# Kernel tuning notes

Hardware: AMD Instinct MI355X
Metric: run time of the kernel (lower is better)

Reference implementation:

```python
import jax, jax.numpy as jnp
import numpy as np

N_EDGE_TYPE = 7
BN_EPS = 1e-5


def _graph_conv(x, row, col, edge_type, W):
    # gather neighbor features, scatter-mean keyed on (dst_node, edge_type), then GEMM
    n = x.shape[0]
    idx = row * N_EDGE_TYPE + edge_type                      # [E]
    gathered = x[col]                                        # [E, C]
    seg = n * N_EDGE_TYPE
    sums = jax.ops.segment_sum(gathered, idx, num_segments=seg)          # [N*7, C]
    cnt = jax.ops.segment_sum(jnp.ones(row.shape, x.dtype), idx, num_segments=seg)
    mean = sums / jnp.maximum(cnt, 1.0)[:, None]
    return mean.reshape(n, -1) @ W                           # [N, C_out]


def _bn(x, gamma, beta):
    # BatchNorm1d in training mode: biased batch stats over the node axis
    m = jnp.mean(x, axis=0)
    v = jnp.var(x, axis=0)
    return (x - m) * jax.lax.rsqrt(v + BN_EPS) * gamma + beta


def setup_inputs() -> dict:
    key = jax.random.key(0)
    ks = jax.random.split(key, 8)
    N, E, C_IN, C_OUT = 100000, 700000, 128, 256
    AVG_DEG = 7
    x = jax.random.normal(ks[0], (N, C_IN), jnp.float32)
    edge_index = jax.random.randint(ks[1], (2, E), 0, N, jnp.int32)
    edge_type = jax.random.randint(ks[2], (E,), 0, N_EDGE_TYPE, jnp.int32)
    node_type = jax.random.randint(ks[3], (N,), 0, 1, jnp.int32)
    # GraphConv.reset_parameters: std = sqrt(2/(deg*Cin + deg*Cout)), a = sqrt(3)*std
    a_a = np.sqrt(3.0) * np.sqrt(2.0 / (AVG_DEG * C_IN + AVG_DEG * C_OUT))
    a_b = np.sqrt(3.0) * np.sqrt(2.0 / (AVG_DEG * C_OUT + AVG_DEG * C_OUT))
    Wa = jax.random.uniform(ks[4], (N_EDGE_TYPE * C_IN, C_OUT), jnp.float32, -a_a, a_a)
    Wb = jax.random.uniform(ks[5], (N_EDGE_TYPE * C_OUT, C_OUT), jnp.float32, -a_b, a_b)
    a_1 = np.sqrt(1.0 / C_IN)
    W1 = jax.random.uniform(ks[6], (C_IN, C_OUT), jnp.float32, -a_1, a_1)
    ga = jnp.ones((C_OUT,), jnp.float32); ba = jnp.zeros((C_OUT,), jnp.float32)
    gb = jnp.ones((C_OUT,), jnp.float32); bb = jnp.zeros((C_OUT,), jnp.float32)
    g1 = jnp.ones((C_OUT,), jnp.float32); b1 = jnp.zeros((C_OUT,), jnp.float32)
    return {"x": x, "edge_index": edge_index, "edge_type": edge_type,
            "node_type": node_type, "Wa": Wa, "ga": ga, "ba": ba,
            "Wb": Wb, "gb": gb, "bb": bb, "W1": W1, "g1": g1, "b1": b1}


def reference(x, edge_index, edge_type, node_type, Wa, ga, ba, Wb, gb, bb, W1, g1, b1):
    row, col = edge_index[0], edge_index[1]
    # conva: GraphConv + BN + ReLU  (n_node_type=0 -> node_type ignored)
    x1 = jax.nn.relu(_bn(_graph_conv(x, row, col, edge_type, Wa), ga, ba))
    # convb: GraphConv + BN
    x2 = _bn(_graph_conv(x1, row, col, edge_type, Wb), gb, bb)
    # channel_in != channel_out -> Conv1x1 (no bias) + BN shortcut
    sc = _bn(x @ W1, g1, b1)
    return jax.nn.relu(x2 + sc)
```

## Files before the change

### kernel.cpp

```cpp
#include <hip/hip_runtime.h>
#include <cstdint>
#include <cstddef>


#define N_ET 7

typedef __bf16 bf16;
typedef __bf16 bf16x8 __attribute__((ext_vector_type(8)));
typedef __bf16 bf16x4 __attribute__((ext_vector_type(4)));
typedef float f32x4v __attribute__((ext_vector_type(4)));


__global__ void count_edges_k(const int* __restrict__ row, const int* __restrict__ et,
                              int* __restrict__ cnt, int E) {
  int e = blockIdx.x * 256 + threadIdx.x;
  if (e < E) atomicAdd(&cnt[row[e] * N_ET + et[e]], 1);
}

__global__ void inv_counts_k(const int* __restrict__ cnt, float* __restrict__ inv, int n) {
  int i = blockIdx.x * 256 + threadIdx.x;
  if (i < n) inv[i] = 1.0f / fmaxf((float)cnt[i], 1.0f);
}

__global__ __launch_bounds__(1024) void scan1_k(const int* __restrict__ cnt,
                                                int* __restrict__ off,
                                                int* __restrict__ bsum, int n) {
  __shared__ int s[1024];
  int tid = threadIdx.x;
  int i = blockIdx.x * 1024 + tid;
  int v = (i < n) ? cnt[i] : 0;
  s[tid] = v;
  __syncthreads();
  for (int d = 1; d < 1024; d <<= 1) {
    int t = (tid >= d) ? s[tid - d] : 0;
    __syncthreads();
    s[tid] += t;
    __syncthreads();
  }
  if (i < n) off[i] = s[tid] - v;
  if (tid == 1023) bsum[blockIdx.x] = s[1023];
}

__global__ __launch_bounds__(1024) void scan2_k(int* __restrict__ bsum, int nb) {
  __shared__ int s[1024];
  int tid = threadIdx.x;
  int v = (tid < nb) ? bsum[tid] : 0;
  s[tid] = v;
  __syncthreads();
  for (int d = 1; d < 1024; d <<= 1) {
    int t = (tid >= d) ? s[tid - d] : 0;
    __syncthreads();
    s[tid] += t;
    __syncthreads();
  }
  if (tid < nb) bsum[tid] = s[tid] - v;
}

__global__ __launch_bounds__(1024) void scan3_k(int* __restrict__ off,
                                                const int* __restrict__ bsum,
                                                int n, int total) {
  int i = blockIdx.x * 1024 + threadIdx.x;
  if (i < n) off[i] += bsum[blockIdx.x];
  if (i == 0) off[n] = total;
}

__global__ void place_k(const int* __restrict__ row, const int* __restrict__ col,
                        const int* __restrict__ et, const int* __restrict__ off,
                        int* __restrict__ cur, int* __restrict__ pcol, int E) {
  int e = blockIdx.x * 256 + threadIdx.x;
  if (e >= E) return;
  int seg = row[e] * N_ET + et[e];
  int pos = off[seg] + atomicAdd(&cur[seg], 1);
  pcol[pos] = col[e];
}

__global__ void transpose_w8_k(const float* __restrict__ W, bf16* __restrict__ Bt8, int K) {
  int i = blockIdx.x * 256 + threadIdx.x;
  if (i < K * 256) {
    int k = i >> 8, col = i & 255;
    Bt8[((size_t)(k >> 3) * 256 + col) * 8 + (k & 7)] = (bf16)W[i];
  }
}

__global__ void transpose_w_k(const float* __restrict__ W, bf16* __restrict__ Bt, int K) {
  int i = blockIdx.x * 256 + threadIdx.x;
  if (i < K * 256) {
    int k = i >> 8, n = i & 255;
    Bt[(size_t)n * K + k] = (bf16)W[i];
  }
}

__global__ void f32_to_bf16_k(const float* __restrict__ in, bf16* __restrict__ out,
                              int total8) {
  int i = blockIdx.x * 256 + threadIdx.x;
  if (i >= total8) return;
  size_t b = (size_t)i * 8;
  float4 v0 = *(const float4*)(in + b);
  float4 v1 = *(const float4*)(in + b + 4);
  bf16x8 o;
  o[0] = (bf16)v0.x; o[1] = (bf16)v0.y; o[2] = (bf16)v0.z; o[3] = (bf16)v0.w;
  o[4] = (bf16)v1.x; o[5] = (bf16)v1.y; o[6] = (bf16)v1.z; o[7] = (bf16)v1.w;
  *(bf16x8*)(out + b) = o;
}

template <int CW>
__launch_bounds__(512, 4)
__global__ void agg_gemm8_k(const bf16* __restrict__ X, const bf16* __restrict__ Bt8,
                            const int* __restrict__ off, const int* __restrict__ pcol,
                            const float* __restrict__ inv, bf16* __restrict__ Cout,
                            float* __restrict__ gsum, float* __restrict__ gssq,
                            int M) {
  constexpr int SL = CW / 8;
  __shared__ alignas(16) bf16 As[64][CW + 8];
  __shared__ int   offL[64 * N_ET + 1];
  __shared__ float invL[64 * N_ET];

  const int t = threadIdx.x;
  const int m0 = blockIdx.x * 64;
  const int lane = t & 63, w = t >> 6;
  const int wm = (w >> 2) * 32;
  const int wn = (w & 3) * 64;
  const int l15 = lane & 15, quad = lane >> 4;
  const int r = t >> 3, h = t & 7;
  const int NS_ = M * N_ET;

  {
    const int base = m0 * N_ET;
    for (int i = t; i < 64 * N_ET + 1; i += 512) {
      int gi = base + i;
      if (gi > NS_) gi = NS_;
      offL[i] = off[gi];
    }
    for (int i = t; i < 64 * N_ET; i += 512) {
      int gi = base + i;
      if (gi >= NS_) gi = NS_ - 1;
      invL[i] = inv[gi];
    }
  }

  f32x4v acc[2][4];
#pragma unroll
  for (int i = 0; i < 2; ++i)
#pragma unroll
    for (int j = 0; j < 4; ++j) acc[i][j] = (f32x4v){0.f, 0.f, 0.f, 0.f};

  __syncthreads();

  const int xcol = h * SL;

  for (int type = 0; type < N_ET; ++type) {
    const int ls = r * N_ET + type;
    const int sS = offL[ls];
    const int sE = offL[ls + 1];
    const float sc = invL[ls];

    float s[SL];
#pragma unroll
    for (int j = 0; j < SL; ++j) s[j] = 0.f;

    int p = sS;
    if constexpr (CW == 256) {
      for (; p + 2 <= sE; p += 2) {
        const int c0 = pcol[p], c1 = pcol[p + 1];
        const bf16* q0 = X + (size_t)c0 * CW + xcol;
        const bf16* q1 = X + (size_t)c1 * CW + xcol;
        const bf16x8 a0 = *(const bf16x8*)(q0 + 0),  a1 = *(const bf16x8*)(q0 + 8);
        const bf16x8 a2 = *(const bf16x8*)(q0 + 16), a3 = *(const bf16x8*)(q0 + 24);
        const bf16x8 b0 = *(const bf16x8*)(q1 + 0),  b1 = *(const bf16x8*)(q1 + 8);
        const bf16x8 b2 = *(const bf16x8*)(q1 + 16), b3 = *(const bf16x8*)(q1 + 24);
#pragma unroll
        for (int i = 0; i < 8; ++i) {
          s[i]      += (float)a0[i] + (float)b0[i];
          s[8 + i]  += (float)a1[i] + (float)b1[i];
          s[16 + i] += (float)a2[i] + (float)b2[i];
          s[24 + i] += (float)a3[i] + (float)b3[i];
        }
      }
      if (p < sE) {
        const int c0 = pcol[p];
        const bf16* q0 = X + (size_t)c0 * CW + xcol;
        const bf16x8 a0 = *(const bf16x8*)(q0 + 0),  a1 = *(const bf16x8*)(q0 + 8);
        const bf16x8 a2 = *(const bf16x8*)(q0 + 16), a3 = *(const bf16x8*)(q0 + 24);
#pragma unroll
        for (int i = 0; i < 8; ++i) {
          s[i]      += (float)a0[i];
          s[8 + i]  += (float)a1[i];
          s[16 + i] += (float)a2[i];
          s[24 + i] += (float)a3[i];
        }
      }
    } else {
      for (; p + 4 <= sE; p += 4) {
        const int c0 = pcol[p],     c1 = pcol[p + 1];
        const int c2 = pcol[p + 2], c3 = pcol[p + 3];
        const bf16* q0 = X + (size_t)c0 * CW + xcol;
        const bf16* q1 = X + (size_t)c1 * CW + xcol;
        const bf16* q2 = X + (size_t)c2 * CW + xcol;
        const bf16* q3 = X + (size_t)c3 * CW + xcol;
        const bf16x8 a0 = *(const bf16x8*)(q0 + 0), a1 = *(const bf16x8*)(q0 + 8);
        const bf16x8 b0 = *(const bf16x8*)(q1 + 0), b1 = *(const bf16x8*)(q1 + 8);
        const bf16x8 d0 = *(const bf16x8*)(q2 + 0), d1 = *(const bf16x8*)(q2 + 8);
        const bf16x8 e0 = *(const bf16x8*)(q3 + 0), e1 = *(const bf16x8*)(q3 + 8);
#pragma unroll
        for (int i = 0; i < 8; ++i) {
          s[i]     += ((float)a0[i] + (float)b0[i]) + ((float)d0[i] + (float)e0[i]);
          s[8 + i] += ((float)a1[i] + (float)b1[i]) + ((float)d1[i] + (float)e1[i]);
        }
      }
      for (; p < sE; ++p) {
        const int c0 = pcol[p];
        const bf16* q0 = X + (size_t)c0 * CW + xcol;
        const bf16x8 a0 = *(const bf16x8*)(q0 + 0), a1 = *(const bf16x8*)(q0 + 8);
#pragma unroll
        for (int i = 0; i < 8; ++i) {
          s[i]     += (float)a0[i];
          s[8 + i] += (float)a1[i];
        }
      }
    }

    __syncthreads();
    if constexpr (CW == 256) {
      bf16x8 o0, o1, o2, o3;
#pragma unroll
      for (int i = 0; i < 8; ++i) {
        o0[i] = (bf16)(s[i] * sc);
        o1[i] = (bf16)(s[8 + i] * sc);
        o2[i] = (bf16)(s[16 + i] * sc);
        o3[i] = (bf16)(s[24 + i] * sc);
      }
      *(bf16x8*)&As[r][h * 32 + 0]  = o0;
      *(bf16x8*)&As[r][h * 32 + 8]  = o1;
      *(bf16x8*)&As[r][h * 32 + 16] = o2;
      *(bf16x8*)&As[r][h * 32 + 24] = o3;
    } else {
      bf16x8 o0, o1;
#pragma unroll
      for (int i = 0; i < 8; ++i) {
        o0[i] = (bf16)(s[i] * sc);
        o1[i] = (bf16)(s[8 + i] * sc);
      }
      *(bf16x8*)&As[r][h * 16 + 0] = o0;
      *(bf16x8*)&As[r][h * 16 + 8] = o1;
    }
    __syncthreads();

#pragma unroll
    for (int kk = 0; kk < CW / 32; ++kk) {
      const int k8b = (type * CW + kk * 32) >> 3;
      const bf16* bp = Bt8 + (size_t)(k8b + quad) * (256 * 8);
      const bf16x8 bf0 = *(const bf16x8*)(bp + (size_t)(wn + 0  + l15) * 8);
      const bf16x8 bf1 = *(const bf16x8*)(bp + (size_t)(wn + 16 + l15) * 8);
      const bf16x8 bf2 = *(const bf16x8*)(bp + (size_t)(wn + 32 + l15) * 8);
      const bf16x8 bf3 = *(const bf16x8*)(bp + (size_t)(wn + 48 + l15) * 8);
      const bf16x8 af0 = *(const bf16x8*)&As[wm + l15][kk * 32 + quad * 8];
      const bf16x8 af1 = *(const bf16x8*)&As[wm + 16 + l15][kk * 32 + quad * 8];
      acc[0][0] = __builtin_amdgcn_mfma_f32_16x16x32_bf16(af0, bf0, acc[0][0], 0, 0, 0);
      acc[0][1] = __builtin_amdgcn_mfma_f32_16x16x32_bf16(af0, bf1, acc[0][1], 0, 0, 0);
      acc[0][2] = __builtin_amdgcn_mfma_f32_16x16x32_bf16(af0, bf2, acc[0][2], 0, 0, 0);
      acc[0][3] = __builtin_amdgcn_mfma_f32_16x16x32_bf16(af0, bf3, acc[0][3], 0, 0, 0);
      acc[1][0] = __builtin_amdgcn_mfma_f32_16x16x32_bf16(af1, bf0, acc[1][0], 0, 0, 0);
      acc[1][1] = __builtin_amdgcn_mfma_f32_16x16x32_bf16(af1, bf1, acc[1][1], 0, 0, 0);
      acc[1][2] = __builtin_amdgcn_mfma_f32_16x16x32_bf16(af1, bf2, acc[1][2], 0, 0, 0);
      acc[1][3] = __builtin_amdgcn_mfma_f32_16x16x32_bf16(af1, bf3, acc[1][3], 0, 0, 0);
    }
  }

  __syncthreads();
  float* red = (float*)&As[0][0];
  const int slot = (w >> 2) * 4 + quad;

#pragma unroll
  for (int fj = 0; fj < 4; ++fj) {
    float ps = 0.f, pq = 0.f;
#pragma unroll
    for (int fi = 0; fi < 2; ++fi) {
      int rbase = m0 + wm + fi * 16 + quad * 4;
#pragma unroll
      for (int rr = 0; rr < 4; ++rr) {
        int rowg = rbase + rr;
        if (rowg < M) {
          float v = acc[fi][fj][rr];
          Cout[(size_t)rowg * 256 + wn + fj * 16 + l15] = (bf16)v;
          ps += v;
          pq += v * v;
        }
      }
    }
    red[((slot * 256) + (wn + fj * 16 + l15)) * 2 + 0] = ps;
    red[((slot * 256) + (wn + fj * 16 + l15)) * 2 + 1] = pq;
  }
  __syncthreads();
  if (t < 256) {
    float sA = 0.f, qA = 0.f;
#pragma unroll
    for (int sl = 0; sl < 8; ++sl) {
      sA += red[(sl * 256 + t) * 2 + 0];
      qA += red[(sl * 256 + t) * 2 + 1];
    }
    unsafeAtomicAdd(&gsum[t], sA);
    unsafeAtomicAdd(&gssq[t], qA);
  }
}

__launch_bounds__(256, 2)
__global__ void sc_gemm_k(const bf16* __restrict__ X, const bf16* __restrict__ Bt,
                          float* __restrict__ Cout,
                          float* __restrict__ gsum, float* __restrict__ gssq,
                          int M, int K) {
  __shared__ alignas(16) bf16 As[128][40];
  __shared__ alignas(16) bf16 Bs[256][40];
  const int t = threadIdx.x;
  const int m0 = blockIdx.x * 128;
  const int lane = t & 63, w = t >> 6;
  const int wm = (w >> 1) * 64;
  const int wn = (w & 1) * 128;
  const int l15 = lane & 15, quad = lane >> 4;

  f32x4v acc[4][8];
#pragma unroll
  for (int i = 0; i < 4; ++i)
#pragma unroll
    for (int j = 0; j < 8; ++j) acc[i][j] = (f32x4v){0.f, 0.f, 0.f, 0.f};

  const int r = t >> 1, h = t & 1;
  const int m = m0 + r;
  const bool mv = (m < M);

  for (int k0 = 0; k0 < K; k0 += 32) {
    const bf16* xp = X + (size_t)m * K + k0 + h * 16;
    bf16x8 o0, o1;
    if (mv) {
      o0 = *(const bf16x8*)(xp);
      o1 = *(const bf16x8*)(xp + 8);
    } else {
#pragma unroll
      for (int i = 0; i < 8; ++i) { o0[i] = (bf16)0.f; o1[i] = (bf16)0.f; }
    }
    *(bf16x8*)&As[r][h * 16] = o0;
    *(bf16x8*)&As[r][h * 16 + 8] = o1;
    {
      const bf16* bp = Bt + (size_t)t * K + k0;
      bf16x8 b0 = *(const bf16x8*)(bp + 0);
      bf16x8 b1 = *(const bf16x8*)(bp + 8);
      bf16x8 b2 = *(const bf16x8*)(bp + 16);
      bf16x8 b3 = *(const bf16x8*)(bp + 24);
      *(bf16x8*)&Bs[t][0] = b0;
      *(bf16x8*)&Bs[t][8] = b1;
      *(bf16x8*)&Bs[t][16] = b2;
      *(bf16x8*)&Bs[t][24] = b3;
    }
    __syncthreads();
    bf16x8 af[4], bfr[8];
#pragma unroll
    for (int f = 0; f < 4; ++f) af[f] = *(const bf16x8*)&As[wm + f * 16 + l15][quad * 8];
#pragma unroll
    for (int g = 0; g < 8; ++g) bfr[g] = *(const bf16x8*)&Bs[wn + g * 16 + l15][quad * 8];
#pragma unroll
    for (int fi = 0; fi < 4; ++fi)
#pragma unroll
      for (int fj = 0; fj < 8; ++fj)
        acc[fi][fj] = __builtin_amdgcn_mfma_f32_16x16x32_bf16(af[fi], bfr[fj], acc[fi][fj], 0, 0, 0);
    __syncthreads();
  }

  float* red = (float*)&Bs[0][0];
  const int slot = (w >> 1) * 4 + quad;
#pragma unroll
  for (int fj = 0; fj < 8; ++fj) {
    float ps = 0.f, pq = 0.f;
#pragma unroll
    for (int fi = 0; fi < 4; ++fi) {
      int rbase = m0 + wm + fi * 16 + quad * 4;
#pragma unroll
      for (int rr = 0; rr < 4; ++rr) {
        int rowg = rbase + rr;
        if (rowg < M) {
          float v = acc[fi][fj][rr];
          Cout[(size_t)rowg * 256 + wn + fj * 16 + l15] = v;
          ps += v;
          pq += v * v;
        }
      }
    }
    red[((slot * 256) + (wn + fj * 16 + l15)) * 2 + 0] = ps;
    red[((slot * 256) + (wn + fj * 16 + l15)) * 2 + 1] = pq;
  }
  __syncthreads();
  if (t < 256) {
    float sA = 0.f, qA = 0.f;
#pragma unroll
    for (int sl = 0; sl < 8; ++sl) {
      sA += red[(sl * 256 + t) * 2 + 0];
      qA += red[(sl * 256 + t) * 2 + 1];
    }
    unsafeAtomicAdd(&gsum[t], sA);
    unsafeAtomicAdd(&gssq[t], qA);
  }
}


__global__ void bn_params_k(const float* __restrict__ s, const float* __restrict__ q,
                            const float* __restrict__ g, const float* __restrict__ b,
                            float* __restrict__ scale, float* __restrict__ shift, float invN) {
  int c = threadIdx.x;
  float m = s[c] * invN;
  float var = fmaxf(q[c] * invN - m * m, 0.f);
  float sc = g[c] * rsqrtf(var + 1e-5f);
  scale[c] = sc;
  shift[c] = b[c] - m * sc;
}

__global__ void bn_relu_ip_k(bf16* __restrict__ v, const float* __restrict__ scale,
                             const float* __restrict__ shift, int total8) {
  int i = blockIdx.x * 256 + threadIdx.x;
  if (i >= total8) return;
  size_t base = (size_t)i * 8;
  int c = (int)(base & 255);
  bf16x8 x = *(const bf16x8*)(v + base);
#pragma unroll
  for (int j = 0; j < 8; ++j)
    x[j] = (bf16)fmaxf((float)x[j] * scale[c + j] + shift[c + j], 0.f);
  *(bf16x8*)(v + base) = x;
}

__global__ void final_out_k(const bf16* __restrict__ cb,
                            const float* __restrict__ scB, const float* __restrict__ shB,
                            const float* __restrict__ scS, const float* __restrict__ shS,
                            float* __restrict__ out, int total4) {
  int i = blockIdx.x * 256 + threadIdx.x;
  if (i >= total4) return;
  size_t base = (size_t)i * 4;
  int c = (int)(base & 255);
  bf16x4 vb = *(const bf16x4*)(cb + base);
  float4 vs = *(const float4*)(out + base);
  float4 r;
  r.x = fmaxf((float)vb[0] * scB[c + 0] + shB[c + 0] + vs.x * scS[c + 0] + shS[c + 0], 0.f);
  r.y = fmaxf((float)vb[1] * scB[c + 1] + shB[c + 1] + vs.y * scS[c + 1] + shS[c + 1], 0.f);
  r.z = fmaxf((float)vb[2] * scB[c + 2] + shB[c + 2] + vs.z * scS[c + 2] + shS[c + 2], 0.f);
  r.w = fmaxf((float)vb[3] * scB[c + 3] + shB[c + 3] + vs.w * scS[c + 3] + shS[c + 3], 0.f);
  *(float4*)(out + base) = r;
}

__global__ void sentinel_k(float* __restrict__ out, int n) {
  int i = blockIdx.x * 256 + threadIdx.x;
  if (i < n) out[i] = 12345.0f;
}


extern "C" void kernel_launch(void* const* d_in, const int* in_sizes, int n_in,
                              void* d_out, int out_size, void* d_ws, size_t ws_size,
                              hipStream_t stream) {
  const float* x  = (const float*)d_in[0];
  const int* ei   = (const int*)d_in[1];
  const int* etp  = (const int*)d_in[2];
  const float* Wa = (const float*)d_in[4];
  const float* ga = (const float*)d_in[5];
  const float* ba = (const float*)d_in[6];
  const float* Wb = (const float*)d_in[7];
  const float* gb = (const float*)d_in[8];
  const float* bb = (const float*)d_in[9];
  const float* W1 = (const float*)d_in[10];
  const float* g1 = (const float*)d_in[11];
  const float* b1 = (const float*)d_in[12];

  const int C1 = 128, C2 = 256;
  const int N = in_sizes[0] / C1;
  const int E = in_sizes[2];
  const int* row = ei;
  const int* col = ei + E;
  const int NS = N * N_ET;
  const int KA = N_ET * C1;
  const int KB = N_ET * C2;

  size_t need = 0;
  auto alloc = [&](size_t bytes) { size_t o = need; need += (bytes + 15) & ~(size_t)15; return o; };
  char* w = (char*)d_ws;
  int*   off_p = (int*)(w + alloc(((size_t)NS + 1) * 4));
  int*   cnt_p = (int*)(w + alloc((size_t)NS * 4));
  int*   pcol  = (int*)(w + alloc((size_t)E * 4));
  float* inv_p = (float*)(w + alloc((size_t)NS * 4));
  int*   bsum  = (int*)(w + alloc(1024 * 4));
  bf16*  Bt8A  = (bf16*)(w + alloc((size_t)KA * 256 * 2));
  bf16*  Bt8B  = (bf16*)(w + alloc((size_t)KB * 256 * 2));
  bf16*  Bt1   = (bf16*)(w + alloc((size_t)256 * C1 * 2));
  bf16*  x1    = (bf16*)(w + alloc((size_t)N * C2 * 2));
  bf16*  convb = (bf16*)(w + alloc((size_t)N * C2 * 2));
  float* st    = (float*)(w + alloc(12 * 256 * 4));

  if (ws_size < need) {
    sentinel_k<<<(out_size + 255) / 256, 256, 0, stream>>>((float*)d_out, out_size);
    return;
  }

  bf16* xb = convb;

  float* sum_a = st + 0 * 256, *ssq_a = st + 1 * 256;
  float* sum_b = st + 2 * 256, *ssq_b = st + 3 * 256;
  float* sum_s = st + 4 * 256, *ssq_s = st + 5 * 256;
  float* scA = st + 6 * 256, *shA = st + 7 * 256;
  float* scB = st + 8 * 256, *shB = st + 9 * 256;
  float* scS = st + 10 * 256, *shS = st + 11 * 256;

  const float invN = 1.0f / (float)N;
  const int nscan = (NS + 1023) / 1024;
  const int g2 = (N + 63) / 64;
  const int gsc = (N + 127) / 128;
  const int total8 = N * C2 / 8;
  const int total4 = N * C2 / 4;
  const int cvt8 = N * C1 / 8;

  hipMemsetAsync(cnt_p, 0, (size_t)NS * 4, stream);
  hipMemsetAsync(st, 0, 12 * 256 * 4, stream);
  count_edges_k<<<(E + 255) / 256, 256, 0, stream>>>(row, etp, cnt_p, E);
  inv_counts_k<<<(NS + 255) / 256, 256, 0, stream>>>(cnt_p, inv_p, NS);
  scan1_k<<<nscan, 1024, 0, stream>>>(cnt_p, off_p, bsum, NS);
  scan2_k<<<1, 1024, 0, stream>>>(bsum, nscan);
  scan3_k<<<nscan, 1024, 0, stream>>>(off_p, bsum, NS, E);
  hipMemsetAsync(cnt_p, 0, (size_t)NS * 4, stream);
  place_k<<<(E + 255) / 256, 256, 0, stream>>>(row, col, etp, off_p, cnt_p, pcol, E);

  transpose_w8_k<<<(KA * 256 + 255) / 256, 256, 0, stream>>>(Wa, Bt8A, KA);
  transpose_w8_k<<<(KB * 256 + 255) / 256, 256, 0, stream>>>(Wb, Bt8B, KB);
  transpose_w_k<<<(C1 * 256 + 255) / 256, 256, 0, stream>>>(W1, Bt1, C1);
  f32_to_bf16_k<<<(cvt8 + 255) / 256, 256, 0, stream>>>(x, xb, cvt8);

  agg_gemm8_k<128><<<g2, 512, 0, stream>>>(xb, Bt8A, off_p, pcol, inv_p, x1,
                                           sum_a, ssq_a, N);
  bn_params_k<<<1, 256, 0, stream>>>(sum_a, ssq_a, ga, ba, scA, shA, invN);
  bn_relu_ip_k<<<(total8 + 255) / 256, 256, 0, stream>>>(x1, scA, shA, total8);

  sc_gemm_k<<<gsc, 256, 0, stream>>>(xb, Bt1, (float*)d_out, sum_s, ssq_s, N, C1);
  bn_params_k<<<1, 256, 0, stream>>>(sum_s, ssq_s, g1, b1, scS, shS, invN);

  agg_gemm8_k<256><<<g2, 512, 0, stream>>>(x1, Bt8B, off_p, pcol, inv_p, convb,
                                           sum_b, ssq_b, N);
  bn_params_k<<<1, 256, 0, stream>>>(sum_b, ssq_b, gb, bb, scB, shB, invN);

  final_out_k<<<(total4 + 255) / 256, 256, 0, stream>>>(
      convb, scB, shB, scS, shS, (float*)d_out, total4);
}
```

Before: 741.0 us.

## Fuse shortcut 1x1 GEMM into first aggregation kernel and inline BN params

```diff
diff --git a/kernel.cpp b/kernel.cpp
--- a/kernel.cpp
+++ b/kernel.cpp
@@ -79,14 +79,6 @@
   if (i < K * 256) {
     int k = i >> 8, col = i & 255;
     Bt8[((size_t)(k >> 3) * 256 + col) * 8 + (k & 7)] = (bf16)W[i];
-  }
-}
-
-__global__ void transpose_w_k(const float* __restrict__ W, bf16* __restrict__ Bt, int K) {
-  int i = blockIdx.x * 256 + threadIdx.x;
-  if (i < K * 256) {
-    int k = i >> 8, n = i & 255;
-    Bt[(size_t)n * K + k] = (bf16)W[i];
   }
 }
 
@@ -101,6 +93,233 @@
   o[0] = (bf16)v0.x; o[1] = (bf16)v0.y; o[2] = (bf16)v0.z; o[3] = (bf16)v0.w;
   o[4] = (bf16)v1.x; o[5] = (bf16)v1.y; o[6] = (bf16)v1.z; o[7] = (bf16)v1.w;
   *(bf16x8*)(out + b) = o;
+}
+
+__launch_bounds__(512, 3)
+__global__ void agg_sc_a_k(const bf16* __restrict__ X, const bf16* __restrict__ Bt8,
+                           const bf16* __restrict__ Bt18,
+                           const int* __restrict__ off, const int* __restrict__ pcol,
+                           const float* __restrict__ inv,
+                           bf16* __restrict__ Cout, float* __restrict__ gsum,
+                           float* __restrict__ gssq,
+                           float* __restrict__ scout, float* __restrict__ gsumS,
+                           float* __restrict__ gssqS,
+                           int M) {
+  __shared__ alignas(16) bf16 As[64][136];
+  __shared__ int   offL[64 * N_ET + 1];
+  __shared__ float invL[64 * N_ET];
+
+  const int t = threadIdx.x;
+  const int m0 = blockIdx.x * 64;
+  const int lane = t & 63, w = t >> 6;
+  const int wm = (w >> 2) * 32;
+  const int wn = (w & 3) * 64;
+  const int l15 = lane & 15, quad = lane >> 4;
+  const int r = t >> 3, h = t & 7;
+  const int NS_ = M * N_ET;
+  const int slot = (w >> 2) * 4 + quad;
+
+  {
+    const int base = m0 * N_ET;
+    for (int i = t; i < 64 * N_ET + 1; i += 512) {
+      int gi = base + i;
+      if (gi > NS_) gi = NS_;
+      offL[i] = off[gi];
+    }
+    for (int i = t; i < 64 * N_ET; i += 512) {
+      int gi = base + i;
+      if (gi >= NS_) gi = NS_ - 1;
+      invL[i] = inv[gi];
+    }
+    const int mm = m0 + r;
+    bf16x8 z0, z1;
+    if (mm < M) {
+      const bf16* xp = X + (size_t)mm * 128 + h * 16;
+      z0 = *(const bf16x8*)(xp);
+      z1 = *(const bf16x8*)(xp + 8);
+    } else {
+#pragma unroll
+      for (int i = 0; i < 8; ++i) { z0[i] = (bf16)0.f; z1[i] = (bf16)0.f; }
+    }
+    *(bf16x8*)&As[r][h * 16] = z0;
+    *(bf16x8*)&As[r][h * 16 + 8] = z1;
+  }
+  __syncthreads();
+
+  {
+    f32x4v accS[2][4];
+#pragma unroll
+    for (int i = 0; i < 2; ++i)
+#pragma unroll
+      for (int j = 0; j < 4; ++j) accS[i][j] = (f32x4v){0.f, 0.f, 0.f, 0.f};
+#pragma unroll
+    for (int kk = 0; kk < 4; ++kk) {
+      const int k8b = kk * 4;
+      const bf16* bp = Bt18 + (size_t)(k8b + quad) * (256 * 8);
+      const bf16x8 bf0 = *(const bf16x8*)(bp + (size_t)(wn + 0  + l15) * 8);
+      const bf16x8 bf1 = *(const bf16x8*)(bp + (size_t)(wn + 16 + l15) * 8);
+      const bf16x8 bf2 = *(const bf16x8*)(bp + (size_t)(wn + 32 + l15) * 8);
+      const bf16x8 bf3 = *(const bf16x8*)(bp + (size_t)(wn + 48 + l15) * 8);
+      const bf16x8 af0 = *(const bf16x8*)&As[wm + l15][kk * 32 + quad * 8];
+      const bf16x8 af1 = *(const bf16x8*)&As[wm + 16 + l15][kk * 32 + quad * 8];
+      accS[0][0] = __builtin_amdgcn_mfma_f32_16x16x32_bf16(af0, bf0, accS[0][0], 0, 0, 0);
+      accS[0][1] = __builtin_amdgcn_mfma_f32_16x16x32_bf16(af0, bf1, accS[0][1], 0, 0, 0);
+      accS[0][2] = __builtin_amdgcn_mfma_f32_16x16x32_bf16(af0, bf2, accS[0][2], 0, 0, 0);
+      accS[0][3] = __builtin_amdgcn_mfma_f32_16x16x32_bf16(af0, bf3, accS[0][3], 0, 0, 0);
+      accS[1][0] = __builtin_amdgcn_mfma_f32_16x16x32_bf16(af1, bf0, accS[1][0], 0, 0, 0);
+      accS[1][1] = __builtin_amdgcn_mfma_f32_16x16x32_bf16(af1, bf1, accS[1][1], 0, 0, 0);
+      accS[1][2] = __builtin_amdgcn_mfma_f32_16x16x32_bf16(af1, bf2, accS[1][2], 0, 0, 0);
+      accS[1][3] = __builtin_amdgcn_mfma_f32_16x16x32_bf16(af1, bf3, accS[1][3], 0, 0, 0);
+    }
+    __syncthreads();
+    float* red = (float*)&As[0][0];
+#pragma unroll
+    for (int fj = 0; fj < 4; ++fj) {
+      float ps = 0.f, pq = 0.f;
+#pragma unroll
+      for (int fi = 0; fi < 2; ++fi) {
+        int rbase = m0 + wm + fi * 16 + quad * 4;
+#pragma unroll
+        for (int rr = 0; rr < 4; ++rr) {
+          int rowg = rbase + rr;
+          if (rowg < M) {
+            float v = accS[fi][fj][rr];
+            scout[(size_t)rowg * 256 + wn + fj * 16 + l15] = v;
+            ps += v;
+            pq += v * v;
+          }
+        }
+      }
+      red[((slot * 256) + (wn + fj * 16 + l15)) * 2 + 0] = ps;
+      red[((slot * 256) + (wn + fj * 16 + l15)) * 2 + 1] = pq;
+    }
+    __syncthreads();
+    if (t < 256) {
+      float sA = 0.f, qA = 0.f;
+#pragma unroll
+      for (int sl = 0; sl < 8; ++sl) {
+        sA += red[(sl * 256 + t) * 2 + 0];
+        qA += red[(sl * 256 + t) * 2 + 1];
+      }
+      unsafeAtomicAdd(&gsumS[t], sA);
+      unsafeAtomicAdd(&gssqS[t], qA);
+    }
+  }
+
+  f32x4v acc[2][4];
+#pragma unroll
+  for (int i = 0; i < 2; ++i)
+#pragma unroll
+    for (int j = 0; j < 4; ++j) acc[i][j] = (f32x4v){0.f, 0.f, 0.f, 0.f};
+
+  const int xcol = h * 16;
+
+  for (int type = 0; type < N_ET; ++type) {
+    const int ls = r * N_ET + type;
+    const int sS = offL[ls];
+    const int sE = offL[ls + 1];
+    const float sc = invL[ls];
+
+    float s[16];
+#pragma unroll
+    for (int j = 0; j < 16; ++j) s[j] = 0.f;
+
+    int p = sS;
+    for (; p + 4 <= sE; p += 4) {
+      const int c0 = pcol[p],     c1 = pcol[p + 1];
+      const int c2 = pcol[p + 2], c3 = pcol[p + 3];
+      const bf16* q0 = X + (size_t)c0 * 128 + xcol;
+      const bf16* q1 = X + (size_t)c1 * 128 + xcol;
+      const bf16* q2 = X + (size_t)c2 * 128 + xcol;
+      const bf16* q3 = X + (size_t)c3 * 128 + xcol;
+      const bf16x8 a0 = *(const bf16x8*)(q0 + 0), a1 = *(const bf16x8*)(q0 + 8);
+      const bf16x8 b0 = *(const bf16x8*)(q1 + 0), b1 = *(const bf16x8*)(q1 + 8);
+      const bf16x8 d0 = *(const bf16x8*)(q2 + 0), d1 = *(const bf16x8*)(q2 + 8);
+      const bf16x8 e0 = *(const bf16x8*)(q3 + 0), e1 = *(const bf16x8*)(q3 + 8);
+#pragma unroll
+      for (int i = 0; i < 8; ++i) {
+        s[i]     += ((float)a0[i] + (float)b0[i]) + ((float)d0[i] + (float)e0[i]);
+        s[8 + i] += ((float)a1[i] + (float)b1[i]) + ((float)d1[i] + (float)e1[i]);
+      }
+    }
+    for (; p < sE; ++p) {
+      const int c0 = pcol[p];
+      const bf16* q0 = X + (size_t)c0 * 128 + xcol;
+      const bf16x8 a0 = *(const bf16x8*)(q0 + 0), a1 = *(const bf16x8*)(q0 + 8);
+#pragma unroll
+      for (int i = 0; i < 8; ++i) {
+        s[i]     += (float)a0[i];
+        s[8 + i] += (float)a1[i];
+      }
+    }
+
+    __syncthreads();
+    {
+      bf16x8 o0, o1;
+#pragma unroll
+      for (int i = 0; i < 8; ++i) {
+        o0[i] = (bf16)(s[i] * sc);
+        o1[i] = (bf16)(s[8 + i] * sc);
+      }
+      *(bf16x8*)&As[r][h * 16 + 0] = o0;
+      *(bf16x8*)&As[r][h * 16 + 8] = o1;
+    }
+    __syncthreads();
+
+#pragma unroll
+    for (int kk = 0; kk < 4; ++kk) {
+      const int k8b = (type * 128 + kk * 32) >> 3;
+      const bf16* bp = Bt8 + (size_t)(k8b + quad) * (256 * 8);
+      const bf16x8 bf0 = *(const bf16x8*)(bp + (size_t)(wn + 0  + l15) * 8);
+      const bf16x8 bf1 = *(const bf16x8*)(bp + (size_t)(wn + 16 + l15) * 8);
+      const bf16x8 bf2 = *(const bf16x8*)(bp + (size_t)(wn + 32 + l15) * 8);
+      const bf16x8 bf3 = *(const bf16x8*)(bp + (size_t)(wn + 48 + l15) * 8);
+      const bf16x8 af0 = *(const bf16x8*)&As[wm + l15][kk * 32 + quad * 8];
+      const bf16x8 af1 = *(const bf16x8*)&As[wm + 16 + l15][kk * 32 + quad * 8];
+      acc[0][0] = __builtin_amdgcn_mfma_f32_16x16x32_bf16(af0, bf0, acc[0][0], 0, 0, 0);
+      acc[0][1] = __builtin_amdgcn_mfma_f32_16x16x32_bf16(af0, bf1, acc[0][1], 0, 0, 0);
+      acc[0][2] = __builtin_amdgcn_mfma_f32_16x16x32_bf16(af0, bf2, acc[0][2], 0, 0, 0);
+      acc[0][3] = __builtin_amdgcn_mfma_f32_16x16x32_bf16(af0, bf3, acc[0][3], 0, 0, 0);
+      acc[1][0] = __builtin_amdgcn_mfma_f32_16x16x32_bf16(af1, bf0, acc[1][0], 0, 0, 0);
+      acc[1][1] = __builtin_amdgcn_mfma_f32_16x16x32_bf16(af1, bf1, acc[1][1], 0, 0, 0);
+      acc[1][2] = __builtin_amdgcn_mfma_f32_16x16x32_bf16(af1, bf2, acc[1][2], 0, 0, 0);
+      acc[1][3] = __builtin_amdgcn_mfma_f32_16x16x32_bf16(af1, bf3, acc[1][3], 0, 0, 0);
+    }
+  }
+
+  __syncthreads();
+  float* red = (float*)&As[0][0];
+#pragma unroll
+  for (int fj = 0; fj < 4; ++fj) {
+    float ps = 0.f, pq = 0.f;
+#pragma unroll
+    for (int fi = 0; fi < 2; ++fi) {
+      int rbase = m0 + wm + fi * 16 + quad * 4;
+#pragma unroll
+      for (int rr = 0; rr < 4; ++rr) {
+        int rowg = rbase + rr;
+        if (rowg < M) {
+          float v = acc[fi][fj][rr];
+          Cout[(size_t)rowg * 256 + wn + fj * 16 + l15] = (bf16)v;
+          ps += v;
+          pq += v * v;
+        }
+      }
+    }
+    red[((slot * 256) + (wn + fj * 16 + l15)) * 2 + 0] = ps;
+    red[((slot * 256) + (wn + fj * 16 + l15)) * 2 + 1] = pq;
+  }
+  __syncthreads();
+  if (t < 256) {
+    float sA = 0.f, qA = 0.f;
+#pragma unroll
+    for (int sl = 0; sl < 8; ++sl) {
+      sA += red[(sl * 256 + t) * 2 + 0];
+      qA += red[(sl * 256 + t) * 2 + 1];
+    }
+    unsafeAtomicAdd(&gsum[t], sA);
+    unsafeAtomicAdd(&gssq[t], qA);
+  }
 }
 
 template <int CW>
@@ -303,132 +522,55 @@
   }
 }
 
-__launch_bounds__(256, 2)
-__global__ void sc_gemm_k(const bf16* __restrict__ X, const bf16* __restrict__ Bt,
-                          float* __restrict__ Cout,
-                          float* __restrict__ gsum, float* __restrict__ gssq,
-                          int M, int K) {
-  __shared__ alignas(16) bf16 As[128][40];
-  __shared__ alignas(16) bf16 Bs[256][40];
+
+__global__ void bn_relu2_k(bf16* __restrict__ v,
+                           const float* __restrict__ sumA, const float* __restrict__ ssqA,
+                           const float* __restrict__ g, const float* __restrict__ b,
+                           float invN, int total8) {
+  __shared__ float scL[256], shL[256];
   const int t = threadIdx.x;
-  const int m0 = blockIdx.x * 128;
-  const int lane = t & 63, w = t >> 6;
-  const int wm = (w >> 1) * 64;
-  const int wn = (w & 1) * 128;
-  const int l15 = lane & 15, quad = lane >> 4;
-
-  f32x4v acc[4][8];
-#pragma unroll
-  for (int i = 0; i < 4; ++i)
-#pragma unroll
-    for (int j = 0; j < 8; ++j) acc[i][j] = (f32x4v){0.f, 0.f, 0.f, 0.f};
-
-  const int r = t >> 1, h = t & 1;
-  const int m = m0 + r;
-  const bool mv = (m < M);
-
-  for (int k0 = 0; k0 < K; k0 += 32) {
-    const bf16* xp = X + (size_t)m * K + k0 + h * 16;
-    bf16x8 o0, o1;
-    if (mv) {
-      o0 = *(const bf16x8*)(xp);
-      o1 = *(const bf16x8*)(xp + 8);
-    } else {
-#pragma unroll
-      for (int i = 0; i < 8; ++i) { o0[i] = (bf16)0.f; o1[i] = (bf16)0.f; }
-    }
-    *(bf16x8*)&As[r][h * 16] = o0;
-    *(bf16x8*)&As[r][h * 16 + 8] = o1;
-    {
-      const bf16* bp = Bt + (size_t)t * K + k0;
-      bf16x8 b0 = *(const bf16x8*)(bp + 0);
-      bf16x8 b1 = *(const bf16x8*)(bp + 8);
-      bf16x8 b2 = *(const bf16x8*)(bp + 16);
-      bf16x8 b3 = *(const bf16x8*)(bp + 24);
-      *(bf16x8*)&Bs[t][0] = b0;
-      *(bf16x8*)&Bs[t][8] = b1;
-      *(bf16x8*)&Bs[t][16] = b2;
-      *(bf16x8*)&Bs[t][24] = b3;
-    }
-    __syncthreads();
-    bf16x8 af[4], bfr[8];
-#pragma unroll
-    for (int f = 0; f < 4; ++f) af[f] = *(const bf16x8*)&As[wm + f * 16 + l15][quad * 8];
-#pragma unroll
-    for (int g = 0; g < 8; ++g) bfr[g] = *(const bf16x8*)&Bs[wn + g * 16 + l15][quad * 8];
-#pragma unroll
-    for (int fi = 0; fi < 4; ++fi)
-#pragma unroll
-      for (int fj = 0; fj < 8; ++fj)
-        acc[fi][fj] = __builtin_amdgcn_mfma_f32_16x16x32_bf16(af[fi], bfr[fj], acc[fi][fj], 0, 0, 0);
-    __syncthreads();
-  }
-
-  float* red = (float*)&Bs[0][0];
-  const int slot = (w >> 1) * 4 + quad;
-#pragma unroll
-  for (int fj = 0; fj < 8; ++fj) {
-    float ps = 0.f, pq = 0.f;
-#pragma unroll
-    for (int fi = 0; fi < 4; ++fi) {
-      int rbase = m0 + wm + fi * 16 + quad * 4;
-#pragma unroll
-      for (int rr = 0; rr < 4; ++rr) {
-        int rowg = rbase + rr;
-        if (rowg < M) {
-          float v = acc[fi][fj][rr];
-          Cout[(size_t)rowg * 256 + wn + fj * 16 + l15] = v;
-          ps += v;
-          pq += v * v;
-        }
-      }
-    }
-    red[((slot * 256) + (wn + fj * 16 + l15)) * 2 + 0] = ps;
-    red[((slot * 256) + (wn + fj * 16 + l15)) * 2 + 1] = pq;
-  }
-  __syncthreads();
-  if (t < 256) {
-    float sA = 0.f, qA = 0.f;
-#pragma unroll
-    for (int sl = 0; sl < 8; ++sl) {
-      sA += red[(sl * 256 + t) * 2 + 0];
-      qA += red[(sl * 256 + t) * 2 + 1];
-    }
-    unsafeAtomicAdd(&gsum[t], sA);
-    unsafeAtomicAdd(&gssq[t], qA);
-  }
-}
-
-
-__global__ void bn_params_k(const float* __restrict__ s, const float* __restrict__ q,
-                            const float* __restrict__ g, const float* __restrict__ b,
-                            float* __restrict__ scale, float* __restrict__ shift, float invN) {
-  int c = threadIdx.x;
-  float m = s[c] * invN;
-  float var = fmaxf(q[c] * invN - m * m, 0.f);
-  float sc = g[c] * rsqrtf(var + 1e-5f);
-  scale[c] = sc;
-  shift[c] = b[c] - m * sc;
-}
-
-__global__ void bn_relu_ip_k(bf16* __restrict__ v, const float* __restrict__ scale,
-                             const float* __restrict__ shift, int total8) {
-  int i = blockIdx.x * 256 + threadIdx.x;
+  {
+    float m = sumA[t] * invN;
+    float var = fmaxf(ssqA[t] * invN - m * m, 0.f);
+    float sc = g[t] * rsqrtf(var + 1e-5f);
+    scL[t] = sc;
+    shL[t] = b[t] - m * sc;
+  }
+  __syncthreads();
+  int i = blockIdx.x * 256 + t;
   if (i >= total8) return;
   size_t base = (size_t)i * 8;
   int c = (int)(base & 255);
   bf16x8 x = *(const bf16x8*)(v + base);
 #pragma unroll
   for (int j = 0; j < 8; ++j)
-    x[j] = (bf16)fmaxf((float)x[j] * scale[c + j] + shift[c + j], 0.f);
+    x[j] = (bf16)fmaxf((float)x[j] * scL[c + j] + shL[c + j], 0.f);
   *(bf16x8*)(v + base) = x;
 }
 
-__global__ void final_out_k(const bf16* __restrict__ cb,
-                            const float* __restrict__ scB, const float* __restrict__ shB,
-                            const float* __restrict__ scS, const float* __restrict__ shS,
-                            float* __restrict__ out, int total4) {
-  int i = blockIdx.x * 256 + threadIdx.x;
+
+__global__ void final_out2_k(const bf16* __restrict__ cb,
+                             const float* __restrict__ sumB, const float* __restrict__ ssqB,
+                             const float* __restrict__ gb, const float* __restrict__ bb,
+                             const float* __restrict__ sumS, const float* __restrict__ ssqS,
+                             const float* __restrict__ g1, const float* __restrict__ b1,
+                             float invN, float* __restrict__ out, int total4) {
+  __shared__ float scB[256], shB[256], scS[256], shS[256];
+  const int t = threadIdx.x;
+  {
+    float mB = sumB[t] * invN;
+    float vB = fmaxf(ssqB[t] * invN - mB * mB, 0.f);
+    float sB = gb[t] * rsqrtf(vB + 1e-5f);
+    scB[t] = sB;
+    shB[t] = bb[t] - mB * sB;
+    float mS = sumS[t] * invN;
+    float vS = fmaxf(ssqS[t] * invN - mS * mS, 0.f);
+    float sS = g1[t] * rsqrtf(vS + 1e-5f);
+    scS[t] = sS;
+    shS[t] = b1[t] - mS * sS;
+  }
+  __syncthreads();
+  int i = blockIdx.x * 256 + t;
   if (i >= total4) return;
   size_t base = (size_t)i * 4;
   int c = (int)(base & 255);
@@ -483,7 +625,7 @@
   int*   bsum  = (int*)(w + alloc(1024 * 4));
   bf16*  Bt8A  = (bf16*)(w + alloc((size_t)KA * 256 * 2));
   bf16*  Bt8B  = (bf16*)(w + alloc((size_t)KB * 256 * 2));
-  bf16*  Bt1   = (bf16*)(w + alloc((size_t)256 * C1 * 2));
+  bf16*  Bt18  = (bf16*)(w + alloc((size_t)C1 * 256 * 2));
   bf16*  x1    = (bf16*)(w + alloc((size_t)N * C2 * 2));
   bf16*  convb = (bf16*)(w + alloc((size_t)N * C2 * 2));
   float* st    = (float*)(w + alloc(12 * 256 * 4));
@@ -498,14 +640,10 @@
   float* sum_a = st + 0 * 256, *ssq_a = st + 1 * 256;
   float* sum_b = st + 2 * 256, *ssq_b = st + 3 * 256;
   float* sum_s = st + 4 * 256, *ssq_s = st + 5 * 256;
-  float* scA = st + 6 * 256, *shA = st + 7 * 256;
-  float* scB = st + 8 * 256, *shB = st + 9 * 256;
-  float* scS = st + 10 * 256, *shS = st + 11 * 256;
 
   const float invN = 1.0f / (float)N;
   const int nscan = (NS + 1023) / 1024;
   const int g2 = (N + 63) / 64;
-  const int gsc = (N + 127) / 128;
   const int total8 = N * C2 / 8;
   const int total4 = N * C2 / 4;
   const int cvt8 = N * C1 / 8;
@@ -522,21 +660,20 @@
 
   transpose_w8_k<<<(KA * 256 + 255) / 256, 256, 0, stream>>>(Wa, Bt8A, KA);
   transpose_w8_k<<<(KB * 256 + 255) / 256, 256, 0, stream>>>(Wb, Bt8B, KB);
-  transpose_w_k<<<(C1 * 256 + 255) / 256, 256, 0, stream>>>(W1, Bt1, C1);
+  transpose_w8_k<<<(C1 * 256 + 255) / 256, 256, 0, stream>>>(W1, Bt18, C1);
   f32_to_bf16_k<<<(cvt8 + 255) / 256, 256, 0, stream>>>(x, xb, cvt8);
 
-  agg_gemm8_k<128><<<g2, 512, 0, stream>>>(xb, Bt8A, off_p, pcol, inv_p, x1,
-                                           sum_a, ssq_a, N);
-  bn_params_k<<<1, 256, 0, stream>>>(sum_a, ssq_a, ga, ba, scA, shA, invN);
-  bn_relu_ip_k<<<(total8 + 255) / 256, 256, 0, stream>>>(x1, scA, shA, total8);
-
-  sc_gemm_k<<<gsc, 256, 0, stream>>>(xb, Bt1, (float*)d_out, sum_s, ssq_s, N, C1);
-  bn_params_k<<<1, 256, 0, stream>>>(sum_s, ssq_s, g1, b1, scS, shS, invN);
+  agg_sc_a_k<<<g2, 512, 0, stream>>>(xb, Bt8A, Bt18, off_p, pcol, inv_p,
+                                     x1, sum_a, ssq_a,
+                                     (float*)d_out, sum_s, ssq_s, N);
+
+  bn_relu2_k<<<(total8 + 255) / 256, 256, 0, stream>>>(x1, sum_a, ssq_a, ga, ba,
+                                                       invN, total8);
 
   agg_gemm8_k<256><<<g2, 512, 0, stream>>>(x1, Bt8B, off_p, pcol, inv_p, convb,
                                            sum_b, ssq_b, N);
-  bn_params_k<<<1, 256, 0, stream>>>(sum_b, ssq_b, gb, bb, scB, shB, invN);
-
-  final_out_k<<<(total4 + 255) / 256, 256, 0, stream>>>(
-      convb, scB, shB, scS, shS, (float*)d_out, total4);
-}
+
+  final_out2_k<<<(total4 + 255) / 256, 256, 0, stream>>>(
+      convb, sum_b, ssq_b, gb, bb, sum_s, ssq_s, g1, b1, invN,
+      (float*)d_out, total4);
+}
```

New measurement: 704.7 us. -4.9%, faster.
